# Performance work log

Measured on AMD Instinct MI355X. Metric: run time of the kernel, lower is better.

The kernel has to match this reference:

```python
import jax, jax.numpy as jnp
import numpy as np

B, S, D = 1, 2048, 1024
H, HD = 16, 64            # heads, head_dim = D // H
TEN, ED, K = 32, 128, 8   # experts, expert_dim, top_k
DS = 2048                 # shared expert dim
THETA = 10000.0
EPS = 1e-6
RSF = 2.5                 # routed_scaling_factor


def setup_inputs() -> dict:
    key = jax.random.key(0)
    ks = jax.random.split(key, 12)
    s = 0.02
    return {
        "x_input": jax.random.normal(ks[0], (B, S, D), jnp.float32),
        "indices": jax.random.randint(ks[1], (B * S, K), 0, TEN, dtype=jnp.int32),
        "values": jax.random.normal(ks[2], (B * S, K), jnp.float32),
        "w_attn": jax.random.normal(ks[3], (D, 3 * D), jnp.float32) * s,
        "w_attn_o": jax.random.normal(ks[4], (D, D), jnp.float32) * s,
        "attn_norm_w": jnp.ones((D,), jnp.float32),
        "ffn_norm_w": jnp.ones((D,), jnp.float32),
        "ffn_experts": jax.random.normal(ks[5], (3, TEN, D, ED), jnp.float32) * s,
        "keys_w": jax.random.normal(ks[6], (D, TEN), jnp.float32) * s,
        "w_up": jax.random.normal(ks[7], (D, 2 * DS), jnp.float32) * s,
        "w_down": jax.random.normal(ks[8], (DS, D), jnp.float32) * s,
    }


def rmsnorm(x, w):
    return x * jax.lax.rsqrt(jnp.mean(x * x, -1, keepdims=True) + EPS) * w


def l2norm(x):
    # F.normalize(x, dim=-1, eps=EPS)
    n = jnp.sqrt(jnp.sum(x * x, -1, keepdims=True))
    return x / jnp.maximum(n, EPS)


def rope(x):
    # x: [B, H, S, HD]
    t = jnp.arange(x.shape[2], dtype=jnp.float32)
    inv = (1.0 / THETA) ** (jnp.arange(0, HD, 2, dtype=jnp.float32) / HD)
    f = jnp.outer(t, inv)[None, None]  # [1,1,S,HD//2]
    cos, sin = jnp.cos(f), jnp.sin(f)
    x1, x2 = jnp.split(x, 2, -1)
    return jnp.concatenate([x1 * cos + x2 * sin, -x1 * sin + x2 * cos], -1)


def reference(x_input, indices, values, w_attn, w_attn_o, attn_norm_w,
              ffn_norm_w, ffn_experts, keys_w, w_up, w_down):
    # ---- attention block ----
    x = rmsnorm(x_input, attn_norm_w)
    qkv = x @ w_attn  # [B,S,3D]
    xq, xk, xv = jnp.split(qkv, 3, -1)
    to_heads = lambda t: t.reshape(B, S, H, HD).transpose(0, 2, 1, 3)  # b h s a
    xq, xk, xv = to_heads(xq), to_heads(xk), to_heads(xv)
    xq, xk = l2norm(xq), l2norm(xk)  # qk_norm
    xq, xk = rope(xq), rope(xk)
    scores = jnp.einsum('bhqd,bhkd->bhqk', xq, xk) / jnp.sqrt(jnp.float32(HD))
    causal = jnp.tril(jnp.ones((S, S), bool))
    scores = jnp.where(causal, scores, jnp.finfo(scores.dtype).min)
    probs = jax.nn.softmax(scores, -1)
    x_attn = jnp.einsum('bhqk,bhkd->bhqd', probs, xv)
    x_attn = x_attn.transpose(0, 2, 1, 3).reshape(B, S, D)
    x_attn_o = x_attn @ w_attn_o
    x_ffn_input = x_attn_o + x_input

    # ---- router ----
    x_ffn = rmsnorm(x_ffn_input, ffn_norm_w)
    xf = x_ffn.reshape(B * S, D)
    logits = xf @ keys_w  # [T, TEN]
    token_values = jnp.take_along_axis(logits, indices, -1)  # [T, K]
    gates = jax.nn.sigmoid(values + token_values) * RSF

    # ---- grouped-GEMM expert dispatch (dense equivalent: combine is linear in score) ----
    T = B * S
    w_route = jnp.zeros((T, TEN), xf.dtype).at[jnp.arange(T)[:, None], indices].add(gates)
    g = jnp.einsum('td,edh->teh', xf, ffn_experts[0])
    u = jnp.einsum('td,edh->teh', xf, ffn_experts[1])
    h = jax.nn.silu(g) * u * w_route[:, :, None]
    y = jnp.einsum('teh,edh->td', h, ffn_experts[2]).reshape(B, S, D)

    # ---- shared expert (SwiGLU FFN) ----
    x1, x2 = jnp.split(x_ffn @ w_up, 2, -1)
    y_shared = (jax.nn.silu(x1) * x2) @ w_down
    y = y + y_shared
    return y + x_ffn_input
```

## Files before the change

kernel.cpp:

```cpp
#include <hip/hip_runtime.h>
#include <math.h>

#define TOKENS 2048
#define DIM 1024
#define NHEADS 16
#define HEADDIM 64
#define NEXP 32
#define EDIM 128
#define TOPK 8
#define DSHARED 2048
#define RSF_ 2.5f
#define EPS_ 1e-6f

using bf8  = __attribute__((ext_vector_type(8))) short;
using f32x4 = __attribute__((ext_vector_type(4))) float;

__device__ __forceinline__ short f2bf(float f) {
    unsigned u = __float_as_uint(f);
    unsigned r = (u + 0x7fffu + ((u >> 16) & 1u)) >> 16;
    return (short)r;
}
__device__ __forceinline__ float bf2f(short s) {
    return __uint_as_float(((unsigned)(unsigned short)s) << 16);
}

__device__ __forceinline__ void async16(const short* g, const short* l) {
    __builtin_amdgcn_global_load_lds(
        (const __attribute__((address_space(1))) void*)(unsigned long long)g,
        (__attribute__((address_space(3))) void*)(unsigned)(unsigned long long)l,
        16, 0, 0);
}

__global__ __launch_bounds__(256) void rmsnorm_kernel(const float* __restrict__ x,
                                                      const float* __restrict__ w,
                                                      short* __restrict__ out) {
    int row = blockIdx.x;
    const float* xr = x + (long long)row * DIM;
    int t = threadIdx.x;
    float4 xv = ((const float4*)xr)[t];
    float ss = xv.x*xv.x + xv.y*xv.y + xv.z*xv.z + xv.w*xv.w;
    #pragma unroll
    for (int off = 32; off; off >>= 1) ss += __shfl_down(ss, off);
    __shared__ float warps[4];
    if ((t & 63) == 0) warps[t >> 6] = ss;
    __syncthreads();
    float tot = warps[0] + warps[1] + warps[2] + warps[3];
    float scale = rsqrtf(tot / (float)DIM + EPS_);
    float4 wv = ((const float4*)w)[t];
    short4 o;
    o.x = f2bf(xv.x * scale * wv.x);
    o.y = f2bf(xv.y * scale * wv.y);
    o.z = f2bf(xv.z * scale * wv.z);
    o.w = f2bf(xv.w * scale * wv.w);
    ((short4*)(out + (long long)row * DIM))[t] = o;
}

__global__ __launch_bounds__(256) void tconv(const float* __restrict__ in, long long sin,
                                             short* __restrict__ out, long long sout,
                                             int K, int N) {
    in  += (long long)blockIdx.z * sin;
    out += (long long)blockIdx.z * sout;
    __shared__ float t[32][33];
    int n0 = blockIdx.x * 32, k0 = blockIdx.y * 32;
    int tx = threadIdx.x & 31, ty = threadIdx.x >> 5;
    #pragma unroll
    for (int r = ty; r < 32; r += 8)
        t[r][tx] = in[(long long)(k0 + r) * N + n0 + tx];
    __syncthreads();
    #pragma unroll
    for (int r = ty; r < 32; r += 8)
        out[(long long)(n0 + r) * K + k0 + tx] = f2bf(t[tx][r]);
}

__global__ void w2conv(const float* __restrict__ in, short* __restrict__ out) {
    long long i = (long long)blockIdx.x * 256 + threadIdx.x;
    int e = (int)(i >> 17);
    int d = (int)(i >> 7) & 1023;
    int h = (int)(i & 127);
    out[(long long)d * (NEXP * EDIM) + e * EDIM + h] = f2bf(in[i]);
}

__global__ __launch_bounds__(256) void guconv(const float* __restrict__ ex,
                                              short* __restrict__ wgu) {
    int z = blockIdx.z;
    int e = z & 31, hf = z >> 5;
    const float* in = ex + (long long)hf * (NEXP * DIM * EDIM) + (long long)e * (DIM * EDIM);
    short* outp = wgu + (long long)e * (256 * 1024);
    __shared__ float t[32][33];
    int n0 = blockIdx.x * 32, k0 = blockIdx.y * 32;
    int tx = threadIdx.x & 31, ty = threadIdx.x >> 5;
    #pragma unroll
    for (int r = ty; r < 32; r += 8)
        t[r][tx] = in[(long long)(k0 + r) * EDIM + n0 + tx];
    __syncthreads();
    #pragma unroll
    for (int r = ty; r < 32; r += 8) {
        int c = n0 + r;
        int rr = ((c >> 4) << 5) + hf * 16 + (c & 15);
        outp[(long long)rr * 1024 + k0 + tx] = f2bf(t[tx][r]);
    }
}

__global__ __launch_bounds__(256) void upconv(const float* __restrict__ in,
                                              short* __restrict__ outp) {
    __shared__ float t[32][33];
    int n0 = blockIdx.x * 32, k0 = blockIdx.y * 32;
    int tx = threadIdx.x & 31, ty = threadIdx.x >> 5;
    #pragma unroll
    for (int r = ty; r < 32; r += 8)
        t[r][tx] = in[(long long)(k0 + r) * (2 * DSHARED) + n0 + tx];
    __syncthreads();
    #pragma unroll
    for (int r = ty; r < 32; r += 8) {
        int n = n0 + r;
        int hf = n >> 11, c2 = n & 2047;
        int rr = ((c2 >> 7) << 8) + (((c2 & 127) >> 4) << 5) + hf * 16 + (c2 & 15);
        outp[(long long)rr * 1024 + k0 + tx] = f2bf(t[tx][r]);
    }
}

template<int MODE>
__global__ __launch_bounds__(256) void gemm_bf16(const short* __restrict__ A, int lda, long long sA,
                                                 const short* __restrict__ Bt, int ldb, long long sBt,
                                                 void* __restrict__ Cv, int ldc, long long sC,
                                                 int M, int N, int K) {
    int koff = 0, Ksub = K;
    if (MODE >= 3) {
        Ksub = K / gridDim.z;
        koff = blockIdx.z * Ksub;
    } else {
        A  += (long long)blockIdx.z * sA;
        Bt += (long long)blockIdx.z * sBt;
    }
    float* Cf = (float*)Cv;
    short* Cs = (short*)Cv;
    Cf += (long long)blockIdx.z * sC;
    Cs += (long long)blockIdx.z * sC;
    const int m0 = blockIdx.y * 128, n0 = blockIdx.x * 128;
    __shared__ short As[2][128 * 64];
    __shared__ short Bs[2][128 * 64];
    const int tid = threadIdx.x, lane = tid & 63, w = tid >> 6;
    const int wm = (w >> 1) * 64, wn = (w & 1) * 64;
    const int drow = lane >> 3;
    const int dcol = ((lane & 7) ^ drow) * 8;
    const short* ag = A + (long long)(m0 + w * 32 + drow) * lda + koff + dcol;
    const short* bg = Bt + (long long)(n0 + w * 32 + drow) * ldb + koff + dcol;
    f32x4 acc[4][4];
    #pragma unroll
    for (int i = 0; i < 4; ++i)
        #pragma unroll
        for (int j = 0; j < 4; ++j) { f32x4 z = {0.f, 0.f, 0.f, 0.f}; acc[i][j] = z; }
    const int ra = lane & 15, quad = lane >> 4;
    const int fs0 = ((quad + 0) ^ (ra & 7)) * 8;
    const int fs1 = ((quad + 4) ^ (ra & 7)) * 8;

    {
        const short* lA = As[0] + w * 32 * 64;
        const short* lB = Bs[0] + w * 32 * 64;
        #pragma unroll
        for (int c = 0; c < 4; ++c) {
            async16(ag + (long long)(c * 8) * lda, lA + c * 512);
            async16(bg + (long long)(c * 8) * ldb, lB + c * 512);
        }
    }
    int cur = 0;
    for (int k0 = 0; k0 < Ksub; k0 += 64) {
        __syncthreads();
        if (k0 + 64 < Ksub) {
            const int nxt = cur ^ 1;
            const short* lA = As[nxt] + w * 32 * 64;
            const short* lB = Bs[nxt] + w * 32 * 64;
            #pragma unroll
            for (int c = 0; c < 4; ++c) {
                async16(ag + (long long)(c * 8) * lda + k0 + 64, lA + c * 512);
                async16(bg + (long long)(c * 8) * ldb + k0 + 64, lB + c * 512);
            }
        }
        const short* cA = As[cur];
        const short* cB = Bs[cur];
        #pragma unroll
        for (int h = 0; h < 2; ++h) {
            const int fs = h ? fs1 : fs0;
            bf8 af[4], bfv[4];
            #pragma unroll
            for (int i = 0; i < 4; ++i) af[i]  = *(const bf8*)(cA + (wm + i * 16 + ra) * 64 + fs);
            #pragma unroll
            for (int j = 0; j < 4; ++j) bfv[j] = *(const bf8*)(cB + (wn + j * 16 + ra) * 64 + fs);
            #pragma unroll
            for (int i = 0; i < 4; ++i)
                #pragma unroll
                for (int j = 0; j < 4; ++j)
                    acc[i][j] = __builtin_amdgcn_mfma_f32_16x16x32_bf16(af[i], bfv[j], acc[i][j], 0, 0, 0);
        }
        cur ^= 1;
    }
    const int cr = quad * 4, cc = ra;
    #pragma unroll
    for (int i = 0; i < 4; ++i) {
        #pragma unroll
        for (int r = 0; r < 4; ++r) {
            int row = m0 + wm + i * 16 + cr + r;
            long long base = (long long)row * ldc + n0 + wn + cc;
            #pragma unroll
            for (int j = 0; j < 4; ++j) {
                float v = acc[i][j][r];
                if (MODE == 2) Cs[base + j * 16] = f2bf(v);
                if (MODE == 3) Cf[base + j * 16] = v;
                if (MODE == 4) Cf[base + j * 16] = Cf[base + j * 16] + v;
            }
        }
    }
}

template<bool SCALED>
__global__ __launch_bounds__(256) void gemm_act(const short* __restrict__ A, int lda,
                                                const short* __restrict__ Bt, long long sBt,
                                                short* __restrict__ Ct, int ldct,
                                                const float* __restrict__ wr) {
    const short* Bp = Bt + (long long)blockIdx.z * sBt + (long long)blockIdx.x * (256 * 1024);
    const int cb = (blockIdx.z * gridDim.x + blockIdx.x) * 128;
    const int m0 = blockIdx.y * 64;
    __shared__ short As[2][64 * 64];
    __shared__ short Bs[2][256 * 64];
    const int tid = threadIdx.x, lane = tid & 63, w = tid >> 6;
    const int wm = (w >> 1) * 32, wn = (w & 1) * 128;
    const int drow = lane >> 3;
    const int dcol = ((lane & 7) ^ drow) * 8;
    const short* ag = A + (long long)(m0 + w * 16 + drow) * lda + dcol;
    const short* bg = Bp + (long long)(w * 64 + drow) * 1024 + dcol;
    f32x4 acc[2][8];
    #pragma unroll
    for (int i = 0; i < 2; ++i)
        #pragma unroll
        for (int j = 0; j < 8; ++j) { f32x4 z = {0.f, 0.f, 0.f, 0.f}; acc[i][j] = z; }
    const int ra = lane & 15, quad = lane >> 4;
    const int fs0 = ((quad + 0) ^ (ra & 7)) * 8;
    const int fs1 = ((quad + 4) ^ (ra & 7)) * 8;

    {
        const short* lA = As[0] + w * 16 * 64;
        const short* lB = Bs[0] + w * 64 * 64;
        async16(ag, lA);
        async16(ag + (long long)8 * lda, lA + 512);
        #pragma unroll
        for (int c = 0; c < 8; ++c)
            async16(bg + (long long)(c * 8) * 1024, lB + c * 512);
    }
    int cur = 0;
    for (int k0 = 0; k0 < 1024; k0 += 64) {
        __syncthreads();
        if (k0 + 64 < 1024) {
            const int nxt = cur ^ 1;
            const short* lA = As[nxt] + w * 16 * 64;
            const short* lB = Bs[nxt] + w * 64 * 64;
            async16(ag + k0 + 64, lA);
            async16(ag + (long long)8 * lda + k0 + 64, lA + 512);
            #pragma unroll
            for (int c = 0; c < 8; ++c)
                async16(bg + (long long)(c * 8) * 1024 + k0 + 64, lB + c * 512);
        }
        const short* cA = As[cur];
        const short* cB = Bs[cur];
        #pragma unroll
        for (int h = 0; h < 2; ++h) {
            const int fs = h ? fs1 : fs0;
            bf8 af0 = *(const bf8*)(cA + (wm + ra) * 64 + fs);
            bf8 af1 = *(const bf8*)(cA + (wm + 16 + ra) * 64 + fs);
            #pragma unroll
            for (int j = 0; j < 8; ++j) {
                bf8 bv = *(const bf8*)(cB + (wn + j * 16 + ra) * 64 + fs);
                acc[0][j] = __builtin_amdgcn_mfma_f32_16x16x32_bf16(af0, bv, acc[0][j], 0, 0, 0);
                acc[1][j] = __builtin_amdgcn_mfma_f32_16x16x32_bf16(af1, bv, acc[1][j], 0, 0, 0);
            }
        }
        cur ^= 1;
    }
    #pragma unroll
    for (int i = 0; i < 2; ++i)
        #pragma unroll
        for (int r = 0; r < 4; ++r) {
            int token = m0 + wm + i * 16 + quad * 4 + r;
            float scale = SCALED ? wr[token * NEXP + blockIdx.z] : 1.0f;
            #pragma unroll
            for (int jp = 0; jp < 4; ++jp) {
                float g = acc[i][2 * jp][r];
                float u = acc[i][2 * jp + 1][r];
                float v = g / (1.0f + __expf(-g)) * u * scale;
                Ct[(long long)token * ldct + cb + wn / 2 + jp * 16 + ra] = f2bf(v);
            }
        }
}

__global__ void combine4(const float* __restrict__ slices, const float* __restrict__ add,
                         float* __restrict__ dst) {
    long long i = (long long)blockIdx.x * 256 + threadIdx.x;
    const long long S4 = (long long)TOKENS * DIM / 4;
    float4 s = ((const float4*)add)[i];
    #pragma unroll
    for (int c = 0; c < 4; ++c) {
        float4 p = ((const float4*)slices)[c * S4 + i];
        s.x += p.x; s.y += p.y; s.z += p.z; s.w += p.w;
    }
    ((float4*)dst)[i] = s;
}

__global__ __launch_bounds__(256) void combine_rms(const float* __restrict__ slices,
                                                   const float* __restrict__ add,
                                                   const float* __restrict__ w,
                                                   float* __restrict__ xffn,
                                                   short* __restrict__ xf) {
    int row = blockIdx.x, t = threadIdx.x;
    long long i = (long long)row * 256 + t;
    const long long S4 = (long long)TOKENS * DIM / 4;
    float4 s = ((const float4*)add)[i];
    #pragma unroll
    for (int c = 0; c < 4; ++c) {
        float4 p = ((const float4*)slices)[c * S4 + i];
        s.x += p.x; s.y += p.y; s.z += p.z; s.w += p.w;
    }
    ((float4*)xffn)[i] = s;
    float ss = s.x*s.x + s.y*s.y + s.z*s.z + s.w*s.w;
    #pragma unroll
    for (int off = 32; off; off >>= 1) ss += __shfl_down(ss, off);
    __shared__ float warps[4];
    if ((t & 63) == 0) warps[t >> 6] = ss;
    __syncthreads();
    float tot = warps[0] + warps[1] + warps[2] + warps[3];
    float scale = rsqrtf(tot / (float)DIM + EPS_);
    float4 wv = ((const float4*)w)[t];
    short4 o;
    o.x = f2bf(s.x * scale * wv.x);
    o.y = f2bf(s.y * scale * wv.y);
    o.z = f2bf(s.z * scale * wv.z);
    o.w = f2bf(s.w * scale * wv.w);
    ((short4*)(xf + (long long)row * DIM))[t] = o;
}

__global__ __launch_bounds__(256) void qkv_post(const short* __restrict__ qkv,
                                                short* __restrict__ q,
                                                short* __restrict__ k) {
    int lane = threadIdx.x & 63;
    int sh = blockIdx.x * 4 + (threadIdx.x >> 6);
    int s = sh >> 4;
    int h = sh & 15;
    const short* base = qkv + (long long)s * 3 * DIM;
    float qv = bf2f(base[h * HEADDIM + lane]);
    float kv = bf2f(base[DIM + h * HEADDIM + lane]);
    float qs = qv * qv, ks = kv * kv;
    #pragma unroll
    for (int off = 32; off; off >>= 1) {
        qs += __shfl_xor(qs, off);
        ks += __shfl_xor(ks, off);
    }
    qv /= fmaxf(sqrtf(qs), EPS_);
    kv /= fmaxf(sqrtf(ks), EPS_);
    int i = lane & 31;
    float f = (float)s * powf(10000.0f, -(float)i / 32.0f);
    float c = cosf(f), sn = sinf(f);
    float qo = __shfl_xor(qv, 32);
    float ko = __shfl_xor(kv, 32);
    float sgn = (lane < 32) ? sn : -sn;
    float qr = qv * c + qo * sgn;
    float kr = kv * c + ko * sgn;
    long long o = ((long long)h * TOKENS + s) * HEADDIM + lane;
    q[o] = f2bf(qr);
    k[o] = f2bf(kr);
}

__global__ __launch_bounds__(256) void vtrans(const short* __restrict__ qkv,
                                              short* __restrict__ vt) {
    int h = blockIdx.z;
    int s0 = blockIdx.x * 32, d0 = blockIdx.y * 32;
    __shared__ short t[32][34];
    int tx = threadIdx.x & 31, ty = threadIdx.x >> 5;
    #pragma unroll
    for (int r = ty; r < 32; r += 8)
        t[r][tx] = qkv[(long long)(s0 + r) * (3 * DIM) + 2 * DIM + h * HEADDIM + d0 + tx];
    __syncthreads();
    #pragma unroll
    for (int r = ty; r < 32; r += 8)
        vt[((long long)h * HEADDIM + d0 + r) * TOKENS + s0 + tx] = t[tx][r];
}

#define PLD 68
__global__ __launch_bounds__(256) void attn_kernel(const short* __restrict__ q,
                                                   const short* __restrict__ k,
                                                   const short* __restrict__ vt,
                                                   float* __restrict__ Oacc,
                                                   float* __restrict__ lacc) {
    const int w = threadIdx.x >> 6, lane = threadIdx.x & 63;
    const int col = lane & 15, quad = lane >> 4;
    const int head = blockIdx.x / 80;
    const int t = blockIdx.x % 80;
    int qb, ch;
    if (t < 8)       { qb = t;                ch = 0; }
    else if (t < 24) { qb = 8 + (t - 8) / 2;  ch = (t - 8) % 2; }
    else if (t < 48) { qb = 16 + (t - 24) / 3; ch = (t - 24) % 3; }
    else             { qb = 24 + (t - 48) / 4; ch = (t - 48) % 4; }
    const int nch = qb / 8 + 1;
    const int ntk = qb + 1;
    const int per = (ntk + nch - 1) / nch;
    const int t0 = ch * per;
    const int t1 = (t0 + per < ntk) ? t0 + per : ntk;
    const int qbase = qb * 64 + w * 16;
    __shared__ short Ks[64 * 64];
    __shared__ short Vs[64 * 64];
    __shared__ short Ps[4 * 16 * PLD];
    short* Pw = Ps + w * 16 * PLD;
    const short* kh = k + (long long)head * TOKENS * HEADDIM;
    const short* vh = vt + (long long)head * HEADDIM * TOKENS;
    const int r8 = lane >> 3;
    const int sw = ((lane & 7) ^ r8) * 8;
    bf8 qf[2];
    #pragma unroll
    for (int ks = 0; ks < 2; ++ks)
        qf[ks] = *(const bf8*)(q + ((long long)head * TOKENS + qbase + col) * HEADDIM + ks * 32 + quad * 8);
    const int fo0 = (((0 * 4) + quad) ^ (col & 7)) * 8;
    const int fo1 = (((1 * 4) + quad) ^ (col & 7)) * 8;
    f32x4 o_[4];
    float l_[4];
    #pragma unroll
    for (int n = 0; n < 4; ++n) { f32x4 z = {0.f, 0.f, 0.f, 0.f}; o_[n] = z; }
    #pragma unroll
    for (int r = 0; r < 4; ++r) l_[r] = 0.f;
    for (int kt = t0; kt < t1; ++kt) {
        const int j0 = kt * 64;
        #pragma unroll
        for (int c = 0; c < 2; ++c) {
            int row = w * 16 + c * 8 + r8;
            async16(kh + (long long)(j0 + row) * HEADDIM + sw, Ks + (w * 16 + c * 8) * 64 + lane * 8);
            async16(vh + (long long)row * TOKENS + j0 + sw, Vs + (w * 16 + c * 8) * 64 + lane * 8);
        }
        __syncthreads();
        f32x4 sacc[4];
        #pragma unroll
        for (int n = 0; n < 4; ++n) { f32x4 z = {0.f, 0.f, 0.f, 0.f}; sacc[n] = z; }
        #pragma unroll
        for (int ks = 0; ks < 2; ++ks) {
            const int fo = ks ? fo1 : fo0;
            #pragma unroll
            for (int nt = 0; nt < 4; ++nt) {
                bf8 kf = *(const bf8*)(Ks + (nt * 16 + col) * 64 + fo);
                sacc[nt] = __builtin_amdgcn_mfma_f32_16x16x32_bf16(qf[ks], kf, sacc[nt], 0, 0, 0);
            }
        }
        const bool diag = (j0 + 64 > qbase);
        #pragma unroll
        for (int nt = 0; nt < 4; ++nt)
            #pragma unroll
            for (int r = 0; r < 4; ++r) {
                float p = __expf(sacc[nt][r] * 0.125f);
                if (diag && (j0 + nt * 16 + col > qbase + quad * 4 + r)) p = 0.f;
                l_[r] += p;
                Pw[(quad * 4 + r) * PLD + nt * 16 + col] = f2bf(p);
            }
        #pragma unroll
        for (int ks = 0; ks < 2; ++ks) {
            bf8 pf = *(const bf8*)(Pw + col * PLD + ks * 32 + quad * 8);
            const int fo = ks ? fo1 : fo0;
            #pragma unroll
            for (int nt = 0; nt < 4; ++nt) {
                bf8 vf = *(const bf8*)(Vs + (nt * 16 + col) * 64 + fo);
                o_[nt] = __builtin_amdgcn_mfma_f32_16x16x32_bf16(pf, vf, o_[nt], 0, 0, 0);
            }
        }
        __syncthreads();
    }
    float* Oc = Oacc + (long long)ch * (TOKENS * DIM);
    #pragma unroll
    for (int r = 0; r < 4; ++r) {
        int row = qbase + quad * 4 + r;
        float* op = Oc + (long long)row * DIM + head * HEADDIM;
        #pragma unroll
        for (int nt = 0; nt < 4; ++nt)
            op[nt * 16 + col] = o_[nt][r];
        float l = l_[r];
        #pragma unroll
        for (int off = 1; off < 16; off <<= 1) l += __shfl_xor(l, off);
        if (col == 0) lacc[ch * (TOKENS * NHEADS) + row * NHEADS + head] = l;
    }
}

__global__ void attn_norm(const float* __restrict__ Oacc, const float* __restrict__ lacc,
                          short* __restrict__ xo) {
    long long i = (long long)blockIdx.x * 256 + threadIdx.x;
    int row = (int)(i >> 10), col = (int)(i & 1023);
    int nch = (row >> 9) + 1;
    int head = col >> 6;
    float so = 0.f, sl = 0.f;
    for (int c = 0; c < nch; ++c) {
        so += Oacc[(long long)c * (TOKENS * DIM) + i];
        sl += lacc[c * (TOKENS * NHEADS) + row * NHEADS + head];
    }
    xo[i] = f2bf(so / sl);
}

__global__ __launch_bounds__(256) void router_kernel(const short* __restrict__ xf,
                                                     const float* __restrict__ keys_w,
                                                     const int* __restrict__ idx,
                                                     const float* __restrict__ vals,
                                                     float* __restrict__ w_route) {
    int t = blockIdx.x;
    int tid = threadIdx.x;
    int e = tid & 31, c = tid >> 5;
    const short* xr = xf + (long long)t * DIM;
    float p = 0.f;
    for (int j = 0; j < 128; ++j)
        p += bf2f(xr[c * 128 + j]) * keys_w[(c * 128 + j) * NEXP + e];
    __shared__ float part[8][32];
    part[c][e] = p;
    __syncthreads();
    if (tid < NEXP) {
        float lg = 0.f;
        #pragma unroll
        for (int cc = 0; cc < 8; ++cc) lg += part[cc][tid];
        part[0][tid] = lg;
    }
    __syncthreads();
    __shared__ float gate_s[TOPK];
    __shared__ int idx_s[TOPK];
    if (tid < TOPK) {
        int ii = idx[t * TOPK + tid];
        float g = vals[t * TOPK + tid] + part[0][ii];
        gate_s[tid] = (1.0f / (1.0f + __expf(-g))) * RSF_;
        idx_s[tid] = ii;
    }
    __syncthreads();
    if (tid < NEXP) {
        float wr = 0.f;
        #pragma unroll
        for (int kk = 0; kk < TOPK; ++kk)
            if (idx_s[kk] == tid) wr += gate_s[kk];
        w_route[(long long)t * NEXP + tid] = wr;
    }
}

extern "C" void kernel_launch(void* const* d_in, const int* in_sizes, int n_in,
                              void* d_out, int out_size, void* d_ws, size_t ws_size,
                              hipStream_t stream) {
    (void)in_sizes; (void)n_in; (void)out_size; (void)ws_size;
    const float* x_input     = (const float*)d_in[0];
    const int*   indices     = (const int*)d_in[1];
    const float* values      = (const float*)d_in[2];
    const float* w_attn      = (const float*)d_in[3];
    const float* w_attn_o    = (const float*)d_in[4];
    const float* attn_norm_w = (const float*)d_in[5];
    const float* ffn_norm_w  = (const float*)d_in[6];
    const float* ffn_experts = (const float*)d_in[7];
    const float* keys_w      = (const float*)d_in[8];
    const float* w_up        = (const float*)d_in[9];
    const float* w_down      = (const float*)d_in[10];
    float* out = (float*)d_out;
    float* ws  = (float*)d_ws;

    const long long M1 = 1024 * 1024;
    const long long SLICE = (long long)TOKENS * DIM;
    float* xffn    = ws + 0 * M1;
    short* xa_bf   = (short*)(ws + 4 * M1);
    short* xf_bf   = (short*)(ws + 4 * M1 + M1 / 2);
    short* xattn_bf= (short*)(ws + 5 * M1);
    float* w_route = ws + 5 * M1 + M1 / 2;
    float* Oacc    = ws + 6 * M1;
    float* lacc    = ws + 14 * M1;
    short* qh_bf   = (short*)(ws + 15 * M1);
    short* kh_bf   = (short*)(ws + 15 * M1 + M1 / 2);
    short* vt_bf   = (short*)(ws + 16 * M1);
    short* wattn_t = (short*)(ws + 17 * M1);
    short* wattno_t= (short*)(ws + 18 * M1 + M1 / 2);
    short* qkv_bf  = (short*)(ws + 21 * M1);
    float* oslice  = ws + 6 * M1;
    short* wgu     = (short*)(ws + 6 * M1);
    short* h_bf    = (short*)(ws + 10 * M1);
    short* w2t     = (short*)(ws + 14 * M1);
    float* yslice  = ws + 16 * M1;
    short* wupt    = (short*)(ws + 6 * M1);
    short* hs_bf   = (short*)(ws + 8 * M1);
    short* wdownt  = (short*)(ws + 10 * M1);

    tconv<<<dim3(3072 / 32, DIM / 32, 1), 256, 0, stream>>>(w_attn, 0, wattn_t, 0, DIM, 3 * DIM);
    rmsnorm_kernel<<<TOKENS, 256, 0, stream>>>(x_input, attn_norm_w, xa_bf);
    gemm_bf16<2><<<dim3(3072 / 128, TOKENS / 128, 1), 256, 0, stream>>>(
        xa_bf, DIM, 0, wattn_t, DIM, 0, qkv_bf, 3 * DIM, 0, TOKENS, 3 * DIM, DIM);
    qkv_post<<<(TOKENS * NHEADS) / 4, 256, 0, stream>>>(qkv_bf, qh_bf, kh_bf);
    vtrans<<<dim3(TOKENS / 32, HEADDIM / 32, NHEADS), 256, 0, stream>>>(qkv_bf, vt_bf);
    attn_kernel<<<NHEADS * 80, 256, 0, stream>>>(qh_bf, kh_bf, vt_bf, Oacc, lacc);
    attn_norm<<<(TOKENS * DIM) / 256, 256, 0, stream>>>(Oacc, lacc, xattn_bf);
    tconv<<<dim3(DIM / 32, DIM / 32, 1), 256, 0, stream>>>(w_attn_o, 0, wattno_t, 0, DIM, DIM);
    gemm_bf16<3><<<dim3(DIM / 128, TOKENS / 128, 4), 256, 0, stream>>>(
        xattn_bf, DIM, 0, wattno_t, DIM, 0, oslice, DIM, SLICE, TOKENS, DIM, DIM);
    combine_rms<<<TOKENS, 256, 0, stream>>>(oslice, x_input, ffn_norm_w, xffn, xf_bf);

    router_kernel<<<TOKENS, 256, 0, stream>>>(xf_bf, keys_w, indices, values, w_route);
    guconv<<<dim3(EDIM / 32, DIM / 32, 2 * NEXP), 256, 0, stream>>>(ffn_experts, wgu);
    gemm_act<true><<<dim3(1, TOKENS / 64, NEXP), 256, 0, stream>>>(
        xf_bf, DIM, wgu, 256 * 1024, h_bf, NEXP * EDIM, w_route);
    w2conv<<<(NEXP * DIM * EDIM) / 256, 256, 0, stream>>>(
        ffn_experts + 2LL * NEXP * DIM * EDIM, w2t);
    gemm_bf16<3><<<dim3(DIM / 128, TOKENS / 128, 4), 256, 0, stream>>>(
        h_bf, NEXP * EDIM, 0, w2t, NEXP * EDIM, 0, yslice, DIM, SLICE, TOKENS, DIM, NEXP * EDIM);

    upconv<<<dim3((2 * DSHARED) / 32, DIM / 32, 1), 256, 0, stream>>>(w_up, wupt);
    gemm_act<false><<<dim3((2 * DSHARED) / 256, TOKENS / 64, 1), 256, 0, stream>>>(
        xf_bf, DIM, wupt, 0, hs_bf, DSHARED, nullptr);
    tconv<<<dim3(DIM / 32, DSHARED / 32, 1), 256, 0, stream>>>(w_down, 0, wdownt, 0, DSHARED, DIM);
    gemm_bf16<4><<<dim3(DIM / 128, TOKENS / 128, 4), 256, 0, stream>>>(
        hs_bf, DSHARED, 0, wdownt, DSHARED, 0, yslice, DIM, SLICE, TOKENS, DIM, DSHARED);

    combine4<<<(TOKENS * DIM) / 1024, 256, 0, stream>>>(yslice, xffn, out);
}
```

Baseline: 395.6 us.

## Replace dense all-expert MoE with sparse bucketed grouped GEMM over routed pairs

Instead of computing gate/up projections for every token against all 32 experts and scaling by a dense route weight, tokens are bucketed per expert (count, prefix, scatter kernels), and grouped GEMMs run only on the routed (token, expert) pairs. The down projection writes per-top-k slot slices, which are summed with the shared-expert output in an 8-way combine. This cuts the expert FLOPs by roughly a factor of four but adds gather-based loads, several small bucketing kernels, and a larger final reduction over eight slices.

```diff
diff --git a/kernel.cpp b/kernel.cpp
--- a/kernel.cpp
+++ b/kernel.cpp
@@ -11,6 +11,8 @@
 #define DSHARED 2048
 #define RSF_ 2.5f
 #define EPS_ 1e-6f
+#define NPAIR (TOKENS * TOPK)
+#define MAXTILES 288
 
 using bf8  = __attribute__((ext_vector_type(8))) short;
 using f32x4 = __attribute__((ext_vector_type(4))) float;
@@ -72,12 +74,12 @@
         out[(long long)(n0 + r) * K + k0 + tx] = f2bf(t[tx][r]);
 }
 
-__global__ void w2conv(const float* __restrict__ in, short* __restrict__ out) {
+__global__ void w2copy(const float* __restrict__ in, short* __restrict__ out) {
     long long i = (long long)blockIdx.x * 256 + threadIdx.x;
-    int e = (int)(i >> 17);
-    int d = (int)(i >> 7) & 1023;
-    int h = (int)(i & 127);
-    out[(long long)d * (NEXP * EDIM) + e * EDIM + h] = f2bf(in[i]);
+    float4 v = ((const float4*)in)[i];
+    short4 o;
+    o.x = f2bf(v.x); o.y = f2bf(v.y); o.z = f2bf(v.z); o.w = f2bf(v.w);
+    ((short4*)out)[i] = o;
 }
 
 __global__ __launch_bounds__(256) void guconv(const float* __restrict__ ex,
@@ -153,7 +155,6 @@
     const int ra = lane & 15, quad = lane >> 4;
     const int fs0 = ((quad + 0) ^ (ra & 7)) * 8;
     const int fs1 = ((quad + 4) ^ (ra & 7)) * 8;
-
     {
         const short* lA = As[0] + w * 32 * 64;
         const short* lB = Bs[0] + w * 32 * 64;
@@ -206,7 +207,6 @@
                 float v = acc[i][j][r];
                 if (MODE == 2) Cs[base + j * 16] = f2bf(v);
                 if (MODE == 3) Cf[base + j * 16] = v;
-                if (MODE == 4) Cf[base + j * 16] = Cf[base + j * 16] + v;
             }
         }
     }
@@ -236,7 +236,6 @@
     const int ra = lane & 15, quad = lane >> 4;
     const int fs0 = ((quad + 0) ^ (ra & 7)) * 8;
     const int fs1 = ((quad + 4) ^ (ra & 7)) * 8;
-
     {
         const short* lA = As[0] + w * 16 * 64;
         const short* lB = Bs[0] + w * 64 * 64;
@@ -291,13 +290,212 @@
         }
 }
 
-__global__ void combine4(const float* __restrict__ slices, const float* __restrict__ add,
+__global__ __launch_bounds__(256) void gemm_gu(const short* __restrict__ A,
+                                               const short* __restrict__ Wgu,
+                                               const int* __restrict__ pairs,
+                                               const int* __restrict__ meta,
+                                               const float* __restrict__ gates,
+                                               short* __restrict__ H) {
+    __shared__ int ts[33];
+    const int tid = threadIdx.x;
+    if (tid < 33) ts[tid] = meta[64 + tid];
+    __syncthreads();
+    const int tile = blockIdx.y;
+    if (tile >= ts[32]) return;
+    int e = 0;
+    while (ts[e + 1] <= tile) ++e;
+    const int off = meta[e];
+    const int cnt = meta[e + 1] - off;
+    const int m0 = (tile - ts[e]) * 64;
+    const int lane = tid & 63, w = tid >> 6;
+    __shared__ int tok_s[64];
+    __shared__ float gt_s[64];
+    if (tid < 64) {
+        int lr = m0 + tid;
+        int pid = pairs[off + (lr < cnt ? lr : 0)];
+        tok_s[tid] = pid >> 3;
+        gt_s[tid] = gates[pid];
+    }
+    __shared__ short As_[2][64 * 64];
+    __shared__ short Bs_[2][128 * 64];
+    const int wm = (w >> 1) * 32, wn = (w & 1) * 64;
+    const int drow = lane >> 3;
+    const int dcol = ((lane & 7) ^ drow) * 8;
+    __syncthreads();
+    const short* ag0 = A + (long long)tok_s[w * 16 + drow] * DIM + dcol;
+    const short* ag1 = A + (long long)tok_s[w * 16 + 8 + drow] * DIM + dcol;
+    const short* bg = Wgu + (long long)e * (256 * 1024)
+                    + (long long)(blockIdx.x * 128 + w * 32 + drow) * 1024 + dcol;
+    f32x4 acc[2][4];
+    #pragma unroll
+    for (int i = 0; i < 2; ++i)
+        #pragma unroll
+        for (int j = 0; j < 4; ++j) { f32x4 z = {0.f, 0.f, 0.f, 0.f}; acc[i][j] = z; }
+    const int ra = lane & 15, quad = lane >> 4;
+    const int fs0 = ((quad + 0) ^ (ra & 7)) * 8;
+    const int fs1 = ((quad + 4) ^ (ra & 7)) * 8;
+    {
+        const short* lA = As_[0] + w * 16 * 64;
+        const short* lB = Bs_[0] + w * 32 * 64;
+        async16(ag0, lA);
+        async16(ag1, lA + 512);
+        #pragma unroll
+        for (int c = 0; c < 4; ++c)
+            async16(bg + (long long)(c * 8) * 1024, lB + c * 512);
+    }
+    int cur = 0;
+    for (int k0 = 0; k0 < 1024; k0 += 64) {
+        __syncthreads();
+        if (k0 + 64 < 1024) {
+            const int nxt = cur ^ 1;
+            const short* lA = As_[nxt] + w * 16 * 64;
+            const short* lB = Bs_[nxt] + w * 32 * 64;
+            async16(ag0 + k0 + 64, lA);
+            async16(ag1 + k0 + 64, lA + 512);
+            #pragma unroll
+            for (int c = 0; c < 4; ++c)
+                async16(bg + (long long)(c * 8) * 1024 + k0 + 64, lB + c * 512);
+        }
+        const short* cA = As_[cur];
+        const short* cB = Bs_[cur];
+        #pragma unroll
+        for (int h2 = 0; h2 < 2; ++h2) {
+            const int fs = h2 ? fs1 : fs0;
+            bf8 af[2], bfv[4];
+            #pragma unroll
+            for (int i = 0; i < 2; ++i) af[i] = *(const bf8*)(cA + (wm + i * 16 + ra) * 64 + fs);
+            #pragma unroll
+            for (int j = 0; j < 4; ++j) bfv[j] = *(const bf8*)(cB + (wn + j * 16 + ra) * 64 + fs);
+            #pragma unroll
+            for (int i = 0; i < 2; ++i)
+                #pragma unroll
+                for (int j = 0; j < 4; ++j)
+                    acc[i][j] = __builtin_amdgcn_mfma_f32_16x16x32_bf16(af[i], bfv[j], acc[i][j], 0, 0, 0);
+        }
+        cur ^= 1;
+    }
+    const int xb = blockIdx.x * 64;
+    #pragma unroll
+    for (int i = 0; i < 2; ++i)
+        #pragma unroll
+        for (int r = 0; r < 4; ++r) {
+            int lr = wm + i * 16 + quad * 4 + r;
+            bool valid = (m0 + lr) < cnt;
+            float gate = gt_s[lr];
+            #pragma unroll
+            for (int jp = 0; jp < 2; ++jp) {
+                float g = acc[i][2 * jp][r];
+                float u = acc[i][2 * jp + 1][r];
+                float v = g / (1.0f + __expf(-g)) * u * gate;
+                if (valid)
+                    H[(long long)(off + m0 + lr) * EDIM + xb + wn / 2 + jp * 16 + ra] = f2bf(v);
+            }
+        }
+}
+
+__global__ __launch_bounds__(256) void gemm_down(const short* __restrict__ H,
+                                                 const short* __restrict__ W2,
+                                                 const int* __restrict__ pairs,
+                                                 const int* __restrict__ meta,
+                                                 float* __restrict__ esl) {
+    __shared__ int ts[33];
+    const int tid = threadIdx.x;
+    if (tid < 33) ts[tid] = meta[64 + tid];
+    __syncthreads();
+    const int tile = blockIdx.y;
+    if (tile >= ts[32]) return;
+    int e = 0;
+    while (ts[e + 1] <= tile) ++e;
+    const int off = meta[e];
+    const int cnt = meta[e + 1] - off;
+    const int m0 = (tile - ts[e]) * 64;
+    const int n0 = blockIdx.x * 128;
+    const int lane = tid & 63, w = tid >> 6;
+    __shared__ int pid_s[64];
+    if (tid < 64) {
+        int lr = m0 + tid;
+        pid_s[tid] = pairs[off + (lr < cnt ? lr : 0)];
+    }
+    __shared__ short As_[2][64 * 64];
+    __shared__ short Bs_[2][128 * 64];
+    const int wm = (w >> 1) * 32, wn = (w & 1) * 64;
+    const int drow = lane >> 3;
+    const int dcol = ((lane & 7) ^ drow) * 8;
+    const short* ag = H + (long long)(off + m0 + w * 16 + drow) * EDIM + dcol;
+    const short* bg = W2 + (long long)e * (DIM * EDIM) + (long long)(n0 + w * 32 + drow) * EDIM + dcol;
+    f32x4 acc[2][4];
+    #pragma unroll
+    for (int i = 0; i < 2; ++i)
+        #pragma unroll
+        for (int j = 0; j < 4; ++j) { f32x4 z = {0.f, 0.f, 0.f, 0.f}; acc[i][j] = z; }
+    const int ra = lane & 15, quad = lane >> 4;
+    const int fs0 = ((quad + 0) ^ (ra & 7)) * 8;
+    const int fs1 = ((quad + 4) ^ (ra & 7)) * 8;
+    {
+        const short* lA = As_[0] + w * 16 * 64;
+        const short* lB = Bs_[0] + w * 32 * 64;
+        async16(ag, lA);
+        async16(ag + 8 * EDIM, lA + 512);
+        #pragma unroll
+        for (int c = 0; c < 4; ++c)
+            async16(bg + (long long)(c * 8) * EDIM, lB + c * 512);
+    }
+    int cur = 0;
+    for (int k0 = 0; k0 < EDIM; k0 += 64) {
+        __syncthreads();
+        if (k0 == 0) {
+            const short* lA = As_[1] + w * 16 * 64;
+            const short* lB = Bs_[1] + w * 32 * 64;
+            async16(ag + 64, lA);
+            async16(ag + 8 * EDIM + 64, lA + 512);
+            #pragma unroll
+            for (int c = 0; c < 4; ++c)
+                async16(bg + (long long)(c * 8) * EDIM + 64, lB + c * 512);
+        }
+        const short* cA = As_[cur];
+        const short* cB = Bs_[cur];
+        #pragma unroll
+        for (int h2 = 0; h2 < 2; ++h2) {
+            const int fs = h2 ? fs1 : fs0;
+            bf8 af[2], bfv[4];
+            #pragma unroll
+            for (int i = 0; i < 2; ++i) af[i] = *(const bf8*)(cA + (wm + i * 16 + ra) * 64 + fs);
+            #pragma unroll
+            for (int j = 0; j < 4; ++j) bfv[j] = *(const bf8*)(cB + (wn + j * 16 + ra) * 64 + fs);
+            #pragma unroll
+            for (int i = 0; i < 2; ++i)
+                #pragma unroll
+                for (int j = 0; j < 4; ++j)
+                    acc[i][j] = __builtin_amdgcn_mfma_f32_16x16x32_bf16(af[i], bfv[j], acc[i][j], 0, 0, 0);
+        }
+        cur ^= 1;
+    }
+    #pragma unroll
+    for (int i = 0; i < 2; ++i)
+        #pragma unroll
+        for (int r = 0; r < 4; ++r) {
+            int lr = wm + i * 16 + quad * 4 + r;
+            if (m0 + lr >= cnt) continue;
+            int pid = pid_s[lr];
+            int t = pid >> 3, kk = pid & 7;
+            float* dst = esl + (long long)kk * ((long long)TOKENS * DIM)
+                       + (long long)t * DIM + n0 + wn + ra;
+            #pragma unroll
+            for (int j = 0; j < 4; ++j) {
+                float v = acc[i][j][r];
+                if (kk < 2) dst[j * 16] = dst[j * 16] + v;
+                else dst[j * 16] = v;
+            }
+        }
+}
+
+__global__ void combine8(const float* __restrict__ slices, const float* __restrict__ add,
                          float* __restrict__ dst) {
     long long i = (long long)blockIdx.x * 256 + threadIdx.x;
     const long long S4 = (long long)TOKENS * DIM / 4;
     float4 s = ((const float4*)add)[i];
     #pragma unroll
-    for (int c = 0; c < 4; ++c) {
+    for (int c = 0; c < 8; ++c) {
         float4 p = ((const float4*)slices)[c * S4 + i];
         s.x += p.x; s.y += p.y; s.z += p.z; s.w += p.w;
     }
@@ -499,7 +697,7 @@
                                                      const float* __restrict__ keys_w,
                                                      const int* __restrict__ idx,
                                                      const float* __restrict__ vals,
-                                                     float* __restrict__ w_route) {
+                                                     float* __restrict__ gates) {
     int t = blockIdx.x;
     int tid = threadIdx.x;
     int e = tid & 31, c = tid >> 5;
@@ -517,21 +715,73 @@
         part[0][tid] = lg;
     }
     __syncthreads();
-    __shared__ float gate_s[TOPK];
-    __shared__ int idx_s[TOPK];
     if (tid < TOPK) {
         int ii = idx[t * TOPK + tid];
         float g = vals[t * TOPK + tid] + part[0][ii];
-        gate_s[tid] = (1.0f / (1.0f + __expf(-g))) * RSF_;
-        idx_s[tid] = ii;
-    }
-    __syncthreads();
-    if (tid < NEXP) {
-        float wr = 0.f;
-        #pragma unroll
-        for (int kk = 0; kk < TOPK; ++kk)
-            if (idx_s[kk] == tid) wr += gate_s[kk];
-        w_route[(long long)t * NEXP + tid] = wr;
+        gates[t * TOPK + tid] = (1.0f / (1.0f + __expf(-g))) * RSF_;
+    }
+}
+
+__global__ __launch_bounds__(1024) void bucket_count(const int* __restrict__ idx,
+                                                     int* __restrict__ cnt) {
+    int e = blockIdx.x;
+    int tid = threadIdx.x, lane = tid & 63, wv = tid >> 6;
+    __shared__ int wsum[16];
+    int c = 0;
+    for (int p = tid; p < NPAIR; p += 1024) c += (idx[p] == e);
+    #pragma unroll
+    for (int off = 32; off; off >>= 1) c += __shfl_down(c, off);
+    if (lane == 0) wsum[wv] = c;
+    __syncthreads();
+    if (tid == 0) {
+        int s = 0;
+        #pragma unroll
+        for (int i = 0; i < 16; ++i) s += wsum[i];
+        cnt[e] = s;
+    }
+}
+
+__global__ void bucket_prefix(const int* __restrict__ cnt, int* __restrict__ meta) {
+    if (threadIdx.x == 0) {
+        int o = 0, t = 0;
+        for (int e = 0; e < NEXP; ++e) {
+            meta[e] = o;
+            meta[64 + e] = t;
+            o += cnt[e];
+            t += (cnt[e] + 63) >> 6;
+        }
+        meta[NEXP] = o;
+        meta[64 + NEXP] = t;
+    }
+}
+
+__global__ __launch_bounds__(1024) void bucket_scatter(const int* __restrict__ idx,
+                                                       const int* __restrict__ meta,
+                                                       int* __restrict__ pairs) {
+    int e = blockIdx.x;
+    int tid = threadIdx.x, lane = tid & 63, wv = tid >> 6;
+    __shared__ int wbase[16];
+    __shared__ int base_s;
+    if (tid == 0) base_s = meta[e];
+    __syncthreads();
+    for (int c0 = 0; c0 < NPAIR; c0 += 1024) {
+        int p = c0 + tid;
+        bool m = (idx[p] == e);
+        unsigned long long b = __ballot(m);
+        int wpos = __popcll(b & ((1ull << lane) - 1ull));
+        if (lane == 0) wbase[wv] = __popcll(b);
+        __syncthreads();
+        int wb = base_s;
+        for (int i = 0; i < wv; ++i) wb += wbase[i];
+        if (m) pairs[wb + wpos] = p;
+        __syncthreads();
+        if (tid == 0) {
+            int tot = 0;
+            #pragma unroll
+            for (int i = 0; i < 16; ++i) tot += wbase[i];
+            base_s += tot;
+        }
+        __syncthreads();
     }
 }
 
@@ -556,10 +806,14 @@
     const long long M1 = 1024 * 1024;
     const long long SLICE = (long long)TOKENS * DIM;
     float* xffn    = ws + 0 * M1;
+    short* w2s     = (short*)(ws + 2 * M1);
     short* xa_bf   = (short*)(ws + 4 * M1);
     short* xf_bf   = (short*)(ws + 4 * M1 + M1 / 2);
     short* xattn_bf= (short*)(ws + 5 * M1);
-    float* w_route = ws + 5 * M1 + M1 / 2;
+    float* gates   = ws + 5 * M1 + M1 / 2;
+    int*   pairsb  = (int*)(gates + NPAIR);
+    int*   cntb    = pairsb + NPAIR;
+    int*   meta    = cntb + 64;
     float* Oacc    = ws + 6 * M1;
     float* lacc    = ws + 14 * M1;
     short* qh_bf   = (short*)(ws + 15 * M1);
@@ -569,13 +823,12 @@
     short* wattno_t= (short*)(ws + 18 * M1 + M1 / 2);
     short* qkv_bf  = (short*)(ws + 21 * M1);
     float* oslice  = ws + 6 * M1;
-    short* wgu     = (short*)(ws + 6 * M1);
-    short* h_bf    = (short*)(ws + 10 * M1);
-    short* w2t     = (short*)(ws + 14 * M1);
-    float* yslice  = ws + 16 * M1;
-    short* wupt    = (short*)(ws + 6 * M1);
-    short* hs_bf   = (short*)(ws + 8 * M1);
-    short* wdownt  = (short*)(ws + 10 * M1);
+    float* eslice  = ws + 6 * M1;
+    short* wupt    = (short*)(ws + 10 * M1);
+    short* hs_bf   = (short*)(ws + 12 * M1);
+    short* wdownt  = (short*)(ws + 14 * M1);
+    short* wgu     = (short*)(ws + 16 * M1);
+    short* h_cmp   = (short*)(ws + 22 * M1);
 
     tconv<<<dim3(3072 / 32, DIM / 32, 1), 256, 0, stream>>>(w_attn, 0, wattn_t, 0, DIM, 3 * DIM);
     rmsnorm_kernel<<<TOKENS, 256, 0, stream>>>(x_input, attn_norm_w, xa_bf);
@@ -590,21 +843,23 @@
         xattn_bf, DIM, 0, wattno_t, DIM, 0, oslice, DIM, SLICE, TOKENS, DIM, DIM);
     combine_rms<<<TOKENS, 256, 0, stream>>>(oslice, x_input, ffn_norm_w, xffn, xf_bf);
 
-    router_kernel<<<TOKENS, 256, 0, stream>>>(xf_bf, keys_w, indices, values, w_route);
-    guconv<<<dim3(EDIM / 32, DIM / 32, 2 * NEXP), 256, 0, stream>>>(ffn_experts, wgu);
-    gemm_act<true><<<dim3(1, TOKENS / 64, NEXP), 256, 0, stream>>>(
-        xf_bf, DIM, wgu, 256 * 1024, h_bf, NEXP * EDIM, w_route);
-    w2conv<<<(NEXP * DIM * EDIM) / 256, 256, 0, stream>>>(
-        ffn_experts + 2LL * NEXP * DIM * EDIM, w2t);
-    gemm_bf16<3><<<dim3(DIM / 128, TOKENS / 128, 4), 256, 0, stream>>>(
-        h_bf, NEXP * EDIM, 0, w2t, NEXP * EDIM, 0, yslice, DIM, SLICE, TOKENS, DIM, NEXP * EDIM);
+    router_kernel<<<TOKENS, 256, 0, stream>>>(xf_bf, keys_w, indices, values, gates);
+    bucket_count<<<NEXP, 1024, 0, stream>>>(indices, cntb);
+    bucket_prefix<<<1, 64, 0, stream>>>(cntb, meta);
+    bucket_scatter<<<NEXP, 1024, 0, stream>>>(indices, meta, pairsb);
 
     upconv<<<dim3((2 * DSHARED) / 32, DIM / 32, 1), 256, 0, stream>>>(w_up, wupt);
     gemm_act<false><<<dim3((2 * DSHARED) / 256, TOKENS / 64, 1), 256, 0, stream>>>(
         xf_bf, DIM, wupt, 0, hs_bf, DSHARED, nullptr);
     tconv<<<dim3(DIM / 32, DSHARED / 32, 1), 256, 0, stream>>>(w_down, 0, wdownt, 0, DSHARED, DIM);
-    gemm_bf16<4><<<dim3(DIM / 128, TOKENS / 128, 4), 256, 0, stream>>>(
-        hs_bf, DSHARED, 0, wdownt, DSHARED, 0, yslice, DIM, SLICE, TOKENS, DIM, DSHARED);
-
-    combine4<<<(TOKENS * DIM) / 1024, 256, 0, stream>>>(yslice, xffn, out);
-}
+    gemm_bf16<3><<<dim3(DIM / 128, TOKENS / 128, 2), 256, 0, stream>>>(
+        hs_bf, DSHARED, 0, wdownt, DSHARED, 0, eslice, DIM, SLICE, TOKENS, DIM, DSHARED);
+
+    guconv<<<dim3(EDIM / 32, DIM / 32, 2 * NEXP), 256, 0, stream>>>(ffn_experts, wgu);
+    gemm_gu<<<dim3(2, MAXTILES, 1), 256, 0, stream>>>(xf_bf, wgu, pairsb, meta, gates, h_cmp);
+    w2copy<<<(NEXP * DIM * EDIM) / 1024, 256, 0, stream>>>(
+        ffn_experts + 2LL * NEXP * DIM * EDIM, w2s);
+    gemm_down<<<dim3(DIM / 128, MAXTILES, 1), 256, 0, stream>>>(h_cmp, w2s, pairsb, meta, eslice);
+
+    combine8<<<(TOKENS * DIM) / 1024, 256, 0, stream>>>(eslice, xffn, out);
+}
```

Result: slower. 412.1 us (+4.2%).

## Bucket tokens per expert and run sparse gate/up GEMM on routed tokens

Applied to the files above, without the earlier changes.

Adds a bucketing kernel that counts and lists, per expert, the tokens with a nonzero route weight, and zeroes the hidden buffer. A new grouped gate/up GEMM then runs only over those token tiles, gathering rows of the input, instead of the dense all-tokens-by-all-experts GEMM. This cuts the gate/up FLOPs to roughly the top-k fraction. The cost is an extra bucketing pass with a serial prefix scan per expert, gathered loads, and a fixed cap of 288 tiles that may be too small if the routing is skewed.

```diff
diff --git a/kernel.cpp b/kernel.cpp
--- a/kernel.cpp
+++ b/kernel.cpp
@@ -11,6 +11,7 @@
 #define DSHARED 2048
 #define RSF_ 2.5f
 #define EPS_ 1e-6f
+#define MAXTILES 288
 
 using bf8  = __attribute__((ext_vector_type(8))) short;
 using f32x4 = __attribute__((ext_vector_type(4))) float;
@@ -153,7 +154,6 @@
     const int ra = lane & 15, quad = lane >> 4;
     const int fs0 = ((quad + 0) ^ (ra & 7)) * 8;
     const int fs1 = ((quad + 4) ^ (ra & 7)) * 8;
-
     {
         const short* lA = As[0] + w * 32 * 64;
         const short* lB = Bs[0] + w * 32 * 64;
@@ -236,7 +236,6 @@
     const int ra = lane & 15, quad = lane >> 4;
     const int fs0 = ((quad + 0) ^ (ra & 7)) * 8;
     const int fs1 = ((quad + 4) ^ (ra & 7)) * 8;
-
     {
         const short* lA = As[0] + w * 16 * 64;
         const short* lB = Bs[0] + w * 64 * 64;
@@ -287,6 +286,163 @@
                 float u = acc[i][2 * jp + 1][r];
                 float v = g / (1.0f + __expf(-g)) * u * scale;
                 Ct[(long long)token * ldct + cb + wn / 2 + jp * 16 + ra] = f2bf(v);
+            }
+        }
+}
+
+__global__ __launch_bounds__(256) void bucket_zero(const float* __restrict__ wr,
+                                                   int* __restrict__ cnt,
+                                                   int* __restrict__ toks,
+                                                   int4* __restrict__ hz) {
+    const int b = blockIdx.x, tid = threadIdx.x;
+    if (b >= NEXP) {
+        long long i = ((long long)(b - NEXP) * 256 + tid) * 4;
+        int4 z = {0, 0, 0, 0};
+        hz[i] = z; hz[i + 1] = z; hz[i + 2] = z; hz[i + 3] = z;
+        return;
+    }
+    const int e = b, lane = tid & 63, wv = tid >> 6;
+    int myoff = 0, mycnt = 0;
+    for (int t = tid; t < TOKENS; t += 256) {
+        const float* row = wr + (long long)t * NEXP;
+        for (int i = 0; i < e; ++i) myoff += (row[i] != 0.0f);
+        mycnt += (row[e] != 0.0f);
+    }
+    #pragma unroll
+    for (int off2 = 32; off2; off2 >>= 1) {
+        myoff += __shfl_down(myoff, off2);
+        mycnt += __shfl_down(mycnt, off2);
+    }
+    __shared__ int s_off[4], s_cnt[4];
+    __shared__ int base_s;
+    __shared__ int wbase[4];
+    if (lane == 0) { s_off[wv] = myoff; s_cnt[wv] = mycnt; }
+    __syncthreads();
+    if (tid == 0) {
+        base_s = s_off[0] + s_off[1] + s_off[2] + s_off[3];
+        cnt[e] = s_cnt[0] + s_cnt[1] + s_cnt[2] + s_cnt[3];
+    }
+    __syncthreads();
+    for (int t0 = 0; t0 < TOKENS; t0 += 256) {
+        int t = t0 + tid;
+        bool m = wr[(long long)t * NEXP + e] != 0.0f;
+        unsigned long long bl = __ballot(m);
+        int wpos = __popcll(bl & ((1ull << lane) - 1ull));
+        if (lane == 0) wbase[wv] = __popcll(bl);
+        __syncthreads();
+        int wb = base_s;
+        for (int i = 0; i < wv; ++i) wb += wbase[i];
+        if (m) toks[wb + wpos] = t;
+        __syncthreads();
+        if (tid == 0) base_s += wbase[0] + wbase[1] + wbase[2] + wbase[3];
+        __syncthreads();
+    }
+}
+
+__global__ __launch_bounds__(256) void gemm_gu(const short* __restrict__ A,
+                                               const short* __restrict__ Wgu,
+                                               const int* __restrict__ toks,
+                                               const int* __restrict__ cnts,
+                                               const float* __restrict__ wr,
+                                               short* __restrict__ H) {
+    __shared__ int ts[NEXP + 1], os[NEXP + 1];
+    const int tid = threadIdx.x;
+    if (tid == 0) {
+        int t = 0, o = 0;
+        for (int i = 0; i < NEXP; ++i) {
+            ts[i] = t; os[i] = o;
+            int c = cnts[i];
+            t += (c + 63) >> 6;
+            o += c;
+        }
+        ts[NEXP] = t; os[NEXP] = o;
+    }
+    __syncthreads();
+    const int tile = blockIdx.x;
+    if (tile >= ts[NEXP]) return;
+    int e = 0;
+    while (ts[e + 1] <= tile) ++e;
+    const int off = os[e];
+    const int cnt = os[e + 1] - off;
+    const int m0 = (tile - ts[e]) * 64;
+    const int lane = tid & 63, w = tid >> 6;
+    __shared__ int tok_s[64];
+    __shared__ float gt_s[64];
+    if (tid < 64) {
+        int lr = m0 + tid;
+        int tk = toks[off + (lr < cnt ? lr : 0)];
+        tok_s[tid] = tk;
+        gt_s[tid] = wr[(long long)tk * NEXP + e];
+    }
+    __shared__ short As_[2][64 * 64];
+    __shared__ short Bs_[2][256 * 64];
+    const int wm = (w >> 1) * 32, wn = (w & 1) * 128;
+    const int drow = lane >> 3;
+    const int dcol = ((lane & 7) ^ drow) * 8;
+    __syncthreads();
+    const short* ag0 = A + (long long)tok_s[w * 16 + drow] * DIM + dcol;
+    const short* ag1 = A + (long long)tok_s[w * 16 + 8 + drow] * DIM + dcol;
+    const short* bg  = Wgu + (long long)e * (256 * 1024) + (long long)(w * 64 + drow) * 1024 + dcol;
+    f32x4 acc[2][8];
+    #pragma unroll
+    for (int i = 0; i < 2; ++i)
+        #pragma unroll
+        for (int j = 0; j < 8; ++j) { f32x4 z = {0.f, 0.f, 0.f, 0.f}; acc[i][j] = z; }
+    const int ra = lane & 15, quad = lane >> 4;
+    const int fs0 = ((quad + 0) ^ (ra & 7)) * 8;
+    const int fs1 = ((quad + 4) ^ (ra & 7)) * 8;
+    {
+        const short* lA = As_[0] + w * 16 * 64;
+        const short* lB = Bs_[0] + w * 64 * 64;
+        async16(ag0, lA);
+        async16(ag1, lA + 512);
+        #pragma unroll
+        for (int c = 0; c < 8; ++c)
+            async16(bg + (long long)(c * 8) * 1024, lB + c * 512);
+    }
+    int cur = 0;
+    for (int k0 = 0; k0 < 1024; k0 += 64) {
+        __syncthreads();
+        if (k0 + 64 < 1024) {
+            const int nxt = cur ^ 1;
+            const short* lA = As_[nxt] + w * 16 * 64;
+            const short* lB = Bs_[nxt] + w * 64 * 64;
+            async16(ag0 + k0 + 64, lA);
+            async16(ag1 + k0 + 64, lA + 512);
+            #pragma unroll
+            for (int c = 0; c < 8; ++c)
+                async16(bg + (long long)(c * 8) * 1024 + k0 + 64, lB + c * 512);
+        }
+        const short* cA = As_[cur];
+        const short* cB = Bs_[cur];
+        #pragma unroll
+        for (int h = 0; h < 2; ++h) {
+            const int fs = h ? fs1 : fs0;
+            bf8 af0 = *(const bf8*)(cA + (wm + ra) * 64 + fs);
+            bf8 af1 = *(const bf8*)(cA + (wm + 16 + ra) * 64 + fs);
+            #pragma unroll
+            for (int j = 0; j < 8; ++j) {
+                bf8 bv = *(const bf8*)(cB + (wn + j * 16 + ra) * 64 + fs);
+                acc[0][j] = __builtin_amdgcn_mfma_f32_16x16x32_bf16(af0, bv, acc[0][j], 0, 0, 0);
+                acc[1][j] = __builtin_amdgcn_mfma_f32_16x16x32_bf16(af1, bv, acc[1][j], 0, 0, 0);
+            }
+        }
+        cur ^= 1;
+    }
+    #pragma unroll
+    for (int i = 0; i < 2; ++i)
+        #pragma unroll
+        for (int r = 0; r < 4; ++r) {
+            int lr = wm + i * 16 + quad * 4 + r;
+            bool valid = (m0 + lr) < cnt;
+            long long hrow = (long long)tok_s[lr] * (NEXP * EDIM) + e * EDIM;
+            float scale = gt_s[lr];
+            #pragma unroll
+            for (int jp = 0; jp < 4; ++jp) {
+                float g = acc[i][2 * jp][r];
+                float u = acc[i][2 * jp + 1][r];
+                float v = g / (1.0f + __expf(-g)) * u * scale;
+                if (valid) H[hrow + wn / 2 + jp * 16 + ra] = f2bf(v);
             }
         }
 }
@@ -560,6 +716,8 @@
     short* xf_bf   = (short*)(ws + 4 * M1 + M1 / 2);
     short* xattn_bf= (short*)(ws + 5 * M1);
     float* w_route = ws + 5 * M1 + M1 / 2;
+    int*   cntb    = (int*)(w_route + TOKENS * NEXP);
+    int*   toks    = cntb + 32;
     float* Oacc    = ws + 6 * M1;
     float* lacc    = ws + 14 * M1;
     short* qh_bf   = (short*)(ws + 15 * M1);
@@ -591,9 +749,9 @@
     combine_rms<<<TOKENS, 256, 0, stream>>>(oslice, x_input, ffn_norm_w, xffn, xf_bf);
 
     router_kernel<<<TOKENS, 256, 0, stream>>>(xf_bf, keys_w, indices, values, w_route);
+    bucket_zero<<<NEXP + 1024, 256, 0, stream>>>(w_route, cntb, toks, (int4*)h_bf);
     guconv<<<dim3(EDIM / 32, DIM / 32, 2 * NEXP), 256, 0, stream>>>(ffn_experts, wgu);
-    gemm_act<true><<<dim3(1, TOKENS / 64, NEXP), 256, 0, stream>>>(
-        xf_bf, DIM, wgu, 256 * 1024, h_bf, NEXP * EDIM, w_route);
+    gemm_gu<<<MAXTILES, 256, 0, stream>>>(xf_bf, wgu, toks, cntb, w_route, h_bf);
     w2conv<<<(NEXP * DIM * EDIM) / 256, 256, 0, stream>>>(
         ffn_experts + 2LL * NEXP * DIM * EDIM, w2t);
     gemm_bf16<3><<<dim3(DIM / 128, TOKENS / 128, 4), 256, 0, stream>>>(
```

New measurement: 434.3 us. 1.1x slower.
